# Kernel tuning notes

Hardware: AMD Instinct MI355X
Metric: run time of the kernel (lower is better)

Reference implementation:

```python
import jax, jax.numpy as jnp
import numpy as np

B, T, I, H = 64, 256, 512, 1024


def setup_inputs() -> dict:
    key = jax.random.key(0)
    ks = jax.random.split(key, 7)
    sI = 1.0 / np.sqrt(I)
    sH = 1.0 / np.sqrt(H)
    x = jax.random.normal(ks[0], (B, T, I), dtype=jnp.float32)
    # Gate order along axis 0: f, i, c(g), o. Each Linear has weight + bias.
    W_x = jax.random.normal(ks[1], (4, H, I), dtype=jnp.float32) * sI   # Wfx,Wix,Wcx,Wox weights
    b_x = jax.random.normal(ks[2], (4, H), dtype=jnp.float32) * sI      # their biases
    W_h = jax.random.normal(ks[3], (4, H, H), dtype=jnp.float32) * sH   # WfH,WiH,WcH,WoH weights
    b_h = jax.random.normal(ks[4], (4, H), dtype=jnp.float32) * sH      # their biases
    # Bf/Bi/Bc/Bo are nn.Linear(1, H) applied to a constant scalar 1.0:
    # B*(1) = weight[:, 0] + bias  -> just two extra [4, H] bias vectors.
    w_B = jax.random.normal(ks[5], (4, H), dtype=jnp.float32)
    b_B = jax.random.normal(ks[6], (4, H), dtype=jnp.float32)
    return {"x": x, "W_x": W_x, "b_x": b_x, "W_h": W_h, "b_h": b_h, "w_B": w_B, "b_B": b_B}


def reference(x, W_x, b_x, W_h, b_h, w_B, b_B):
    Bb, Tt, Ii = x.shape
    Hh = W_h.shape[-1]
    # All input-dependent gate pre-activations and all static biases, precomputed
    # in one batched GEMM: [B, T, 4, H]
    bias = b_x + b_h + w_B + b_B                     # [4, H]
    xg = jnp.einsum('bti,ghi->btgh', x, W_x) + bias  # [B, T, 4, H]

    h0 = jnp.zeros((Bb, Hh), dtype=x.dtype)
    c0 = jnp.zeros((Bb, Hh), dtype=x.dtype)

    def step(carry, xg_t):
        h, c = carry
        g = xg_t + jnp.einsum('bh,gkh->bgk', h, W_h)  # [B, 4, H]
        f = jax.nn.sigmoid(g[:, 0])
        i = jax.nn.sigmoid(g[:, 1])
        g_c = jnp.tanh(g[:, 2])
        o = jax.nn.sigmoid(g[:, 3])
        c_new = f * c + i * g_c
        h_new = o * jnp.tanh(c_new)
        return (h_new, c_new), h_new

    (_, _), hs = jax.lax.scan(step, (h0, c0), jnp.swapaxes(xg, 0, 1))  # hs: [T, B, H]
    return jnp.swapaxes(hs, 0, 1)  # [B, T, H]
```

## Files before the change

kernel.cpp:

```cpp
#include <hip/hip_runtime.h>
#include <hip/hip_cooperative_groups.h>

namespace cg = cooperative_groups;


using f32x4 = __attribute__((ext_vector_type(4))) float;
using u32x4 = __attribute__((ext_vector_type(4))) unsigned int;

#define NB 64
#define NT 256
#define NI 512
#define NH 1024

#define OFF_WHH  0u
#define SZ_WHH   (4u*1024u*1024u*2u)
#define OFF_WXH  (OFF_WHH + SZ_WHH)
#define SZ_WXH   (4u*1024u*512u*2u)
#define OFF_XH   (OFF_WXH + SZ_WXH)
#define SZ_XH    (256u*64u*512u*2u)
#define OFF_BIAS (OFF_XH + SZ_XH)
#define SZ_BIAS  (4096u*4u)
#define OFF_HG   (OFF_BIAS + SZ_BIAS)
#define SZ_HG    (2u*4u*16u*1024u*2u)
#define OFF_FLG  (OFF_HG + SZ_HG)
#define SZ_FLG   (256u*4u*64u*4u)
#define OFF_XG   (OFF_FLG + SZ_FLG)
#define SZ_XG    (256ull*64ull*4ull*1024ull*2ull)

#define L_H    0
#define L_WX   32768
#define L_ACC_S  98304
#define L_HOUT_S 102656
#define LDS_SLOW 103168
#define L_ACC_F  32768
#define L_HOUT_F 37120
#define LDS_FAST 37632
#define XG_LDS   65536

#define GUARD_PRE(acc)  asm volatile("s_nop 1\ns_nop 1" : "+v"(acc))
#define GUARD_POST(acc) asm volatile("s_nop 7\ns_nop 7\ns_nop 7" : "+v"(acc))

__device__ __forceinline__ unsigned short f2h(float f) {
  _Float16 h = (_Float16)f;
  return __builtin_bit_cast(unsigned short, h);
}
__device__ __forceinline__ float h2f(unsigned short u) {
  _Float16 h = __builtin_bit_cast(_Float16, u);
  return (float)h;
}
__device__ __forceinline__ float sigmoid_f(float x) {
  return 1.0f / (1.0f + __expf(-x));
}
__device__ __forceinline__ float tanh_f(float x) {
  float xc = fminf(fmaxf(x, -15.0f), 15.0f);
  float e = __expf(2.0f * xc);
  return 1.0f - 2.0f / (e + 1.0f);
}


__global__ __launch_bounds__(256) void pack_w_kernel(
    const float* __restrict__ Wh, const float* __restrict__ Wx,
    unsigned short* __restrict__ WhP, unsigned short* __restrict__ WxP) {
  int base = (blockIdx.x * 256 + threadIdx.x) * 4;
  const int nWh = 4 * 1024 * 1024;
  const int nWx = 4 * 1024 * 512;
  if (base < nWh) {
    const float* s = Wh + base;
    unsigned int o0 = (unsigned int)f2h(s[0]) | ((unsigned int)f2h(s[1]) << 16);
    unsigned int o1 = (unsigned int)f2h(s[2]) | ((unsigned int)f2h(s[3]) << 16);
    ((unsigned int*)(WhP + base))[0] = o0;
    ((unsigned int*)(WhP + base))[1] = o1;
  } else {
    int b2 = base - nWh;
    if (b2 < nWx) {
      const float* s = Wx + b2;
      unsigned int o0 = (unsigned int)f2h(s[0]) | ((unsigned int)f2h(s[1]) << 16);
      unsigned int o1 = (unsigned int)f2h(s[2]) | ((unsigned int)f2h(s[3]) << 16);
      ((unsigned int*)(WxP + b2))[0] = o0;
      ((unsigned int*)(WxP + b2))[1] = o1;
    }
  }
}

__global__ __launch_bounds__(256) void pack_x_kernel(
    const float* __restrict__ x, unsigned short* __restrict__ xh) {
  int gid = blockIdx.x * 256 + threadIdx.x;
  int i8 = gid & 63;
  int t  = (gid >> 6) & 255;
  int b  = gid >> 14;
  const float* s = x + (((size_t)b * NT + t) * NI + i8 * 8);
  unsigned int w[4];
#pragma unroll
  for (int j = 0; j < 4; ++j)
    w[j] = (unsigned int)f2h(s[2*j]) | ((unsigned int)f2h(s[2*j+1]) << 16);
  u32x4 v = {w[0], w[1], w[2], w[3]};
  *(u32x4*)(xh + (((size_t)t * NB + b) * NI + i8 * 8)) = v;
}

__global__ __launch_bounds__(256) void prep_small_kernel(
    const float* __restrict__ b_x, const float* __restrict__ b_h,
    const float* __restrict__ w_B, const float* __restrict__ b_B,
    float* __restrict__ bias) {
  int gid = blockIdx.x * 256 + threadIdx.x;
  if (gid < 4096) bias[gid] = b_x[gid] + b_h[gid] + w_B[gid] + b_B[gid];
}


__global__ __launch_bounds__(256) void xg_gemm(
    const unsigned short* __restrict__ Wxh,
    const unsigned short* __restrict__ xh,
    unsigned short* __restrict__ xg) {
  extern __shared__ char smem[];
  const int ug = blockIdx.x & 63;
  const int mc = blockIdx.x >> 6;
  const int tid  = threadIdx.x;
  const int w    = tid >> 6;
  const int l15  = tid & 15;
  const int kg   = (tid & 63) >> 4;

  {
    int r = tid >> 2, seg = tid & 3;
    int gg = r >> 4, uu = r & 15;
    const unsigned short* wsrc = Wxh + ((size_t)(gg * 1024 + ug * 16 + uu)) * 512;
    char* row = smem + r * 1024;
    int sw = (r & 7) << 4;
#pragma unroll
    for (int j = 0; j < 16; ++j) {
      int chunk = seg * 16 + j;
      u32x4 v = *(const u32x4*)(wsrc + chunk * 8);
      *(u32x4*)(row + ((chunk * 16) ^ sw)) = v;
    }
  }
  __syncthreads();

  const int swl = (l15 & 7) << 4;

#pragma unroll 1
  for (int i = 0; i < 4; ++i) {
    const int mt = mc * 16 + w * 4 + i;
    const int t  = mt >> 2;
    const int b0 = (mt & 3) << 4;

    u32x4 xa[16];
    const unsigned short* xp = xh + ((size_t)t * NB + b0 + l15) * NI + kg * 8;
#pragma unroll
    for (int kc = 0; kc < 16; ++kc) xa[kc] = *(const u32x4*)(xp + kc * 32);

#pragma unroll 1
    for (int gg = 0; gg < 4; ++gg) {
      f32x4 acc = {0.0f, 0.0f, 0.0f, 0.0f};
      GUARD_PRE(acc);
      const char* wxrow = smem + (gg * 16 + l15) * 1024;
#pragma unroll
      for (int kc = 0; kc < 16; ++kc) {
        u32x4 b = *(const u32x4*)(wxrow + ((kc * 64 + kg * 16) ^ swl));
        asm("v_mfma_f32_16x16x32_f16 %0, %1, %2, %0" : "+v"(acc) : "v"(xa[kc]), "v"(b));
      }
      GUARD_POST(acc);

#pragma unroll
      for (int r = 0; r < 4; ++r) {
        size_t addr = (((size_t)t * NB + b0 + kg * 4 + r) * 4 + gg) * 1024 + ug * 16 + l15;
        xg[addr] = f2h(acc[r]);
      }
    }
  }
}


__global__ __launch_bounds__(256, 1) void lstm_persist_slow(
    const unsigned short* __restrict__ Whh,
    const unsigned short* __restrict__ Wxh,
    const unsigned short* __restrict__ xh,
    const float* __restrict__ bias,
    unsigned short* __restrict__ hglob,
    unsigned int* __restrict__ flags,
    float* __restrict__ out) {
  extern __shared__ char smem[];
  const int bid  = blockIdx.x;
  const int bt   = bid & 3;
  const int ug   = bid >> 2;
  const int tid  = threadIdx.x;
  const int g    = tid >> 6;
  const int lane = tid & 63;
  const int l15  = lane & 15;
  const int kg   = lane >> 4;

  cg::grid_group grid = cg::this_grid();

  __hip_atomic_store(&flags[bid * 256 + tid], 0u,
                     __ATOMIC_RELAXED, __HIP_MEMORY_SCOPE_AGENT);

  u32x4 bh[32];
  {
    const unsigned short* wr = Whh + ((size_t)(g * 1024 + ug * 16 + l15)) * 1024 + kg * 8;
#pragma unroll
    for (int kc = 0; kc < 32; ++kc) bh[kc] = *(const u32x4*)(wr + kc * 32);
  }
#pragma unroll
  for (int kc = 0; kc < 32; ++kc)
    asm volatile("" : "+v"(bh[kc]));
  {
    int r = tid >> 2, seg = tid & 3;
    int gg = r >> 4, uu = r & 15;
    const unsigned short* wsrc = Wxh + ((size_t)(gg * 1024 + ug * 16 + uu)) * 512;
    char* row = smem + L_WX + r * 1024;
    int sw = (r & 7) << 4;
#pragma unroll
    for (int j = 0; j < 16; ++j) {
      int chunk = seg * 16 + j;
      u32x4 v = *(const u32x4*)(wsrc + chunk * 8);
      *(u32x4*)(row + ((chunk * 16) ^ sw)) = v;
    }
  }
  const float bv = bias[g * 1024 + ug * 16 + l15];
  __syncthreads();

  grid.sync();

  const int eb = tid >> 4;
  const int eu = tid & 15;
  float c_reg = 0.0f;

  float* accl = (float*)(smem + L_ACC_S);
  unsigned short* houtl = (unsigned short*)(smem + L_HOUT_S);

  for (int t = 0; t < NT; ++t) {
    const int buf = t & 1, pbuf = buf ^ 1;

    f32x4 acc = {bv, bv, bv, bv};
    GUARD_PRE(acc);

    {
      const unsigned short* xp = xh + ((size_t)t * NB + bt * 16 + l15) * NI + kg * 8;
      const char* wxrow = smem + L_WX + (g * 16 + l15) * 1024;
      const int sw = (l15 & 7) << 4;
#pragma unroll
      for (int kc = 0; kc < 16; ++kc) {
        u32x4 a = *(const u32x4*)(xp + kc * 32);
        u32x4 b = *(const u32x4*)(wxrow + ((kc * 64 + kg * 16) ^ sw));
        asm("v_mfma_f32_16x16x32_f16 %0, %1, %2, %0" : "+v"(acc) : "v"(a), "v"(b));
      }
    }

    if (t > 0) {
      if (g == 0) {
        const unsigned int* cp = flags + ((t - 1) * 4 + bt) * 64 + lane;
        unsigned int fv;
        while (true) {
          asm volatile("global_load_dword %0, %1, off sc0 sc1\n\ts_waitcnt vmcnt(0)"
                       : "=v"(fv) : "v"(cp) : "memory");
          if (__all(fv == 1u)) break;
          __builtin_amdgcn_s_sleep(2);
        }
      }
      __syncthreads();

      const int sb = tid >> 4, sc = tid & 15;
      const unsigned short* hp = hglob + ((size_t)(pbuf * 4 + bt) * 16 + sb) * 1024 + sc * 8;
      u32x4 v0, v1, v2, v3, v4, v5, v6, v7;
      asm volatile(
          "global_load_dwordx4 %0, %[p], off sc0 sc1\n\t"
          "global_load_dwordx4 %1, %[p], off offset:256 sc0 sc1\n\t"
          "global_load_dwordx4 %2, %[p], off offset:512 sc0 sc1\n\t"
          "global_load_dwordx4 %3, %[p], off offset:768 sc0 sc1\n\t"
          "global_load_dwordx4 %4, %[p], off offset:1024 sc0 sc1\n\t"
          "global_load_dwordx4 %5, %[p], off offset:1280 sc0 sc1\n\t"
          "global_load_dwordx4 %6, %[p], off offset:1536 sc0 sc1\n\t"
          "global_load_dwordx4 %7, %[p], off offset:1792 sc0 sc1\n\t"
          "s_waitcnt vmcnt(0)"
          : "=&v"(v0), "=&v"(v1), "=&v"(v2), "=&v"(v3),
            "=&v"(v4), "=&v"(v5), "=&v"(v6), "=&v"(v7)
          : [p] "v"(hp)
          : "memory");
      char* hrow = smem + L_H + sb * 2048;
      const int sw = (sb & 7) << 4;
      *(u32x4*)(hrow + ((sc * 16 +    0) ^ sw)) = v0;
      *(u32x4*)(hrow + ((sc * 16 +  256) ^ sw)) = v1;
      *(u32x4*)(hrow + ((sc * 16 +  512) ^ sw)) = v2;
      *(u32x4*)(hrow + ((sc * 16 +  768) ^ sw)) = v3;
      *(u32x4*)(hrow + ((sc * 16 + 1024) ^ sw)) = v4;
      *(u32x4*)(hrow + ((sc * 16 + 1280) ^ sw)) = v5;
      *(u32x4*)(hrow + ((sc * 16 + 1536) ^ sw)) = v6;
      *(u32x4*)(hrow + ((sc * 16 + 1792) ^ sw)) = v7;
      __syncthreads();

      const char* hbase = smem + L_H + l15 * 2048;
      const int swh = (l15 & 7) << 4;
#pragma unroll
      for (int kc = 0; kc < 32; ++kc) {
        u32x4 a = *(const u32x4*)(hbase + ((kc * 64 + kg * 16) ^ swh));
        asm("v_mfma_f32_16x16x32_f16 %0, %1, %2, %0" : "+v"(acc) : "v"(a), "v"(bh[kc]));
      }
    }
    GUARD_POST(acc);

#pragma unroll
    for (int r = 0; r < 4; ++r)
      accl[g * 272 + (kg * 4 + r) * 17 + l15] = acc[r];
    __syncthreads();

    {
      float gf = accl[0 * 272 + eb * 17 + eu];
      float gi = accl[1 * 272 + eb * 17 + eu];
      float gc = accl[2 * 272 + eb * 17 + eu];
      float go = accl[3 * 272 + eb * 17 + eu];
      float f  = sigmoid_f(gf);
      float i  = sigmoid_f(gi);
      float cb = tanh_f(gc);
      float o  = sigmoid_f(go);
      float cn = f * c_reg + i * cb;
      c_reg = cn;
      float hn = o * tanh_f(cn);
      out[(((size_t)(bt * 16 + eb)) * NT + t) * NH + ug * 16 + eu] = hn;
      houtl[eb * 16 + eu] = f2h(hn);
    }
    __syncthreads();

    if (t + 1 < NT) {
      if (tid < 32) {
        u32x4 hv = *(const u32x4*)(houtl + tid * 8);
        unsigned short* dst = hglob + ((size_t)(buf * 4 + bt) * 16 + (tid >> 1)) * 1024
                            + ug * 16 + (tid & 1) * 8;
        asm volatile("global_store_dwordx4 %[p], %[v], off sc0 sc1\n\t"
                     "s_waitcnt vmcnt(0)"
                     :: [p] "v"(dst), [v] "v"(hv) : "memory");
      }
      if (tid == 0) {
        unsigned int* fp = flags + (t * 4 + bt) * 64 + ug;
        unsigned int one = 1u;
        asm volatile("global_store_dword %0, %1, off sc0 sc1"
                     :: "v"(fp), "v"(one) : "memory");
      }
    }
  }
}


__global__ __launch_bounds__(256, 1) void lstm_persist_fast(
    const unsigned short* __restrict__ Whh,
    const unsigned short* __restrict__ xg,
    const float* __restrict__ bias,
    unsigned short* __restrict__ hglob,
    unsigned int* __restrict__ flags,
    float* __restrict__ out) {
  extern __shared__ char smem[];
  const int bid  = blockIdx.x;
  const int bt   = bid & 3;
  const int ug   = bid >> 2;
  const int tid  = threadIdx.x;
  const int g    = tid >> 6;
  const int lane = tid & 63;
  const int l15  = lane & 15;
  const int kg   = lane >> 4;

  cg::grid_group grid = cg::this_grid();

  __hip_atomic_store(&flags[bid * 256 + tid], 0u,
                     __ATOMIC_RELAXED, __HIP_MEMORY_SCOPE_AGENT);

  u32x4 bh[32];
  {
    const unsigned short* wr = Whh + ((size_t)(g * 1024 + ug * 16 + l15)) * 1024 + kg * 8;
#pragma unroll
    for (int kc = 0; kc < 32; ++kc) bh[kc] = *(const u32x4*)(wr + kc * 32);
  }
#pragma unroll
  for (int kc = 0; kc < 32; ++kc)
    asm volatile("" : "+v"(bh[kc]));
  const float bv = bias[g * 1024 + ug * 16 + l15];
  __syncthreads();

  grid.sync();

  const int eb = tid >> 4;
  const int eu = tid & 15;
  float c_reg = 0.0f;

  float* accl = (float*)(smem + L_ACC_F);
  unsigned short* houtl = (unsigned short*)(smem + L_HOUT_F);

  const size_t xg_eb = ((size_t)(bt * 16 + eb) * 4) * 1024 + ug * 16 + eu;
  const size_t xg_tstr = (size_t)NB * 4 * 1024;

  for (int t = 0; t < NT; ++t) {
    const int buf = t & 1, pbuf = buf ^ 1;

    const unsigned short* qp = xg + (size_t)t * xg_tstr + xg_eb;
    unsigned short q0 = qp[0];
    unsigned short q1 = qp[1024];
    unsigned short q2 = qp[2048];
    unsigned short q3 = qp[3072];

    f32x4 acc = {bv, bv, bv, bv};
    GUARD_PRE(acc);

    if (t > 0) {
      if (g == 0) {
        const unsigned int* cp = flags + ((t - 1) * 4 + bt) * 64 + lane;
        unsigned int fv;
        while (true) {
          asm volatile("global_load_dword %0, %1, off sc0 sc1\n\ts_waitcnt vmcnt(0)"
                       : "=v"(fv) : "v"(cp) : "memory");
          if (__all(fv == 1u)) break;
          __builtin_amdgcn_s_sleep(2);
        }
      }
      __syncthreads();

      const int sb = tid >> 4, sc = tid & 15;
      const unsigned short* hp = hglob + ((size_t)(pbuf * 4 + bt) * 16 + sb) * 1024 + sc * 8;
      u32x4 v0, v1, v2, v3, v4, v5, v6, v7;
      asm volatile(
          "global_load_dwordx4 %0, %[p], off sc0 sc1\n\t"
          "global_load_dwordx4 %1, %[p], off offset:256 sc0 sc1\n\t"
          "global_load_dwordx4 %2, %[p], off offset:512 sc0 sc1\n\t"
          "global_load_dwordx4 %3, %[p], off offset:768 sc0 sc1\n\t"
          "global_load_dwordx4 %4, %[p], off offset:1024 sc0 sc1\n\t"
          "global_load_dwordx4 %5, %[p], off offset:1280 sc0 sc1\n\t"
          "global_load_dwordx4 %6, %[p], off offset:1536 sc0 sc1\n\t"
          "global_load_dwordx4 %7, %[p], off offset:1792 sc0 sc1\n\t"
          "s_waitcnt vmcnt(0)"
          : "=&v"(v0), "=&v"(v1), "=&v"(v2), "=&v"(v3),
            "=&v"(v4), "=&v"(v5), "=&v"(v6), "=&v"(v7)
          : [p] "v"(hp)
          : "memory");
      char* hrow = smem + L_H + sb * 2048;
      const int sw = (sb & 7) << 4;
      *(u32x4*)(hrow + ((sc * 16 +    0) ^ sw)) = v0;
      *(u32x4*)(hrow + ((sc * 16 +  256) ^ sw)) = v1;
      *(u32x4*)(hrow + ((sc * 16 +  512) ^ sw)) = v2;
      *(u32x4*)(hrow + ((sc * 16 +  768) ^ sw)) = v3;
      *(u32x4*)(hrow + ((sc * 16 + 1024) ^ sw)) = v4;
      *(u32x4*)(hrow + ((sc * 16 + 1280) ^ sw)) = v5;
      *(u32x4*)(hrow + ((sc * 16 + 1536) ^ sw)) = v6;
      *(u32x4*)(hrow + ((sc * 16 + 1792) ^ sw)) = v7;
      __syncthreads();

      const char* hbase = smem + L_H + l15 * 2048;
      const int swh = (l15 & 7) << 4;
#pragma unroll
      for (int kc = 0; kc < 32; ++kc) {
        u32x4 a = *(const u32x4*)(hbase + ((kc * 64 + kg * 16) ^ swh));
        asm("v_mfma_f32_16x16x32_f16 %0, %1, %2, %0" : "+v"(acc) : "v"(a), "v"(bh[kc]));
      }
    }
    GUARD_POST(acc);

#pragma unroll
    for (int r = 0; r < 4; ++r)
      accl[g * 272 + (kg * 4 + r) * 17 + l15] = acc[r];
    __syncthreads();

    {
      float gf = accl[0 * 272 + eb * 17 + eu] + h2f(q0);
      float gi = accl[1 * 272 + eb * 17 + eu] + h2f(q1);
      float gc = accl[2 * 272 + eb * 17 + eu] + h2f(q2);
      float go = accl[3 * 272 + eb * 17 + eu] + h2f(q3);
      float f  = sigmoid_f(gf);
      float i  = sigmoid_f(gi);
      float cb = tanh_f(gc);
      float o  = sigmoid_f(go);
      float cn = f * c_reg + i * cb;
      c_reg = cn;
      float hn = o * tanh_f(cn);
      out[(((size_t)(bt * 16 + eb)) * NT + t) * NH + ug * 16 + eu] = hn;
      houtl[eb * 16 + eu] = f2h(hn);
    }
    __syncthreads();

    if (t + 1 < NT) {
      if (tid < 32) {
        u32x4 hv = *(const u32x4*)(houtl + tid * 8);
        unsigned short* dst = hglob + ((size_t)(buf * 4 + bt) * 16 + (tid >> 1)) * 1024
                            + ug * 16 + (tid & 1) * 8;
        asm volatile("global_store_dwordx4 %[p], %[v], off sc0 sc1\n\t"
                     "s_waitcnt vmcnt(0)"
                     :: [p] "v"(dst), [v] "v"(hv) : "memory");
      }
      if (tid == 0) {
        unsigned int* fp = flags + (t * 4 + bt) * 64 + ug;
        unsigned int one = 1u;
        asm volatile("global_store_dword %0, %1, off sc0 sc1"
                     :: "v"(fp), "v"(one) : "memory");
      }
    }
  }
}


extern "C" void kernel_launch(void* const* d_in, const int* in_sizes, int n_in,
                              void* d_out, int out_size, void* d_ws, size_t ws_size,
                              hipStream_t stream) {
  (void)in_sizes; (void)n_in; (void)out_size;
  const float* x   = (const float*)d_in[0];
  const float* W_x = (const float*)d_in[1];
  const float* b_x = (const float*)d_in[2];
  const float* W_h = (const float*)d_in[3];
  const float* b_h = (const float*)d_in[4];
  const float* w_B = (const float*)d_in[5];
  const float* b_B = (const float*)d_in[6];
  float* out = (float*)d_out;

  char* ws = (char*)d_ws;
  unsigned short* Whh  = (unsigned short*)(ws + OFF_WHH);
  unsigned short* Wxh  = (unsigned short*)(ws + OFF_WXH);
  unsigned short* xhp  = (unsigned short*)(ws + OFF_XH);
  float*          bias = (float*)(ws + OFF_BIAS);
  unsigned short* hg   = (unsigned short*)(ws + OFF_HG);
  unsigned int*   flg  = (unsigned int*)(ws + OFF_FLG);
  unsigned short* xg   = (unsigned short*)(ws + OFF_XG);

  const size_t need_fast = (size_t)OFF_XG + (size_t)SZ_XG;
  const bool fast = (ws_size >= need_fast);

  hipFuncSetAttribute(reinterpret_cast<const void*>(lstm_persist_slow),
                      hipFuncAttributeMaxDynamicSharedMemorySize, LDS_SLOW);
  hipFuncSetAttribute(reinterpret_cast<const void*>(lstm_persist_fast),
                      hipFuncAttributeMaxDynamicSharedMemorySize, LDS_FAST);
  hipFuncSetAttribute(reinterpret_cast<const void*>(xg_gemm),
                      hipFuncAttributeMaxDynamicSharedMemorySize, XG_LDS);

  pack_w_kernel<<<dim3(6144), dim3(256), 0, stream>>>(W_h, W_x, Whh, Wxh);
  pack_x_kernel<<<dim3(4096), dim3(256), 0, stream>>>(x, xhp);
  prep_small_kernel<<<dim3(16), dim3(256), 0, stream>>>(b_x, b_h, w_B, b_B, bias);

  if (fast) {
    xg_gemm<<<dim3(4096), dim3(256), XG_LDS, stream>>>(Wxh, xhp, xg);
    void* kargs[] = {(void*)&Whh, (void*)&xg, (void*)&bias,
                     (void*)&hg, (void*)&flg, (void*)&out};
    hipLaunchCooperativeKernel(reinterpret_cast<void*>(lstm_persist_fast),
                               dim3(256), dim3(256), kargs, LDS_FAST, stream);
  } else {
    void* kargs[] = {(void*)&Whh, (void*)&Wxh, (void*)&xhp, (void*)&bias,
                     (void*)&hg, (void*)&flg, (void*)&out};
    hipLaunchCooperativeKernel(reinterpret_cast<void*>(lstm_persist_slow),
                               dim3(256), dim3(256), kargs, LDS_SLOW, stream);
  }
}
```

Baseline: 1.096 ms.

## Widen xg GEMM tiles to 32 units and split recurrent MFMA accumulator chain

The input-projection GEMM now gives each block 32 hidden units instead of 16, staging 128KB of W_x in LDS and halving the grid, so each loaded x fragment feeds twice as many MFMAs. Separately, the recurrent step in the persistent fast kernel splits its 32-deep MFMA dependency chain across two accumulators that are summed at the end, to shorten the serial MFMA latency on the critical per-timestep path. The larger LDS footprint lowers xg_gemm occupancy, and the two-accumulator sum changes the rounding order slightly.

Measured after the change: 1.184 ms. +8.0%, slower.

```diff
diff --git a/kernel.cpp b/kernel.cpp
--- a/kernel.cpp
+++ b/kernel.cpp
@@ -35,7 +35,7 @@
 #define L_ACC_F  32768
 #define L_HOUT_F 37120
 #define LDS_FAST 37632
-#define XG_LDS   65536
+#define XG_LDS   131072
 
 #define GUARD_PRE(acc)  asm volatile("s_nop 1\ns_nop 1" : "+v"(acc))
 #define GUARD_POST(acc) asm volatile("s_nop 7\ns_nop 7\ns_nop 7" : "+v"(acc))
@@ -111,22 +111,22 @@
     const unsigned short* __restrict__ xh,
     unsigned short* __restrict__ xg) {
   extern __shared__ char smem[];
-  const int ug = blockIdx.x & 63;
-  const int mc = blockIdx.x >> 6;
+  const int ug2 = blockIdx.x & 31;
+  const int mc  = blockIdx.x >> 5;
   const int tid  = threadIdx.x;
   const int w    = tid >> 6;
   const int l15  = tid & 15;
   const int kg   = (tid & 63) >> 4;
 
   {
-    int r = tid >> 2, seg = tid & 3;
-    int gg = r >> 4, uu = r & 15;
-    const unsigned short* wsrc = Wxh + ((size_t)(gg * 1024 + ug * 16 + uu)) * 512;
-    char* row = smem + r * 1024;
-    int sw = (r & 7) << 4;
-#pragma unroll
-    for (int j = 0; j < 16; ++j) {
-      int chunk = seg * 16 + j;
+    int rr = tid >> 1, seg = tid & 1;
+    int gg = rr >> 5, uu = rr & 31;
+    const unsigned short* wsrc = Wxh + ((size_t)(gg * 1024 + ug2 * 32 + uu)) * 512;
+    char* row = smem + rr * 1024;
+    int sw = (rr & 7) << 4;
+#pragma unroll
+    for (int j = 0; j < 32; ++j) {
+      int chunk = seg * 32 + j;
       u32x4 v = *(const u32x4*)(wsrc + chunk * 8);
       *(u32x4*)(row + ((chunk * 16) ^ sw)) = v;
     }
@@ -148,20 +148,24 @@
 
 #pragma unroll 1
     for (int gg = 0; gg < 4; ++gg) {
-      f32x4 acc = {0.0f, 0.0f, 0.0f, 0.0f};
-      GUARD_PRE(acc);
-      const char* wxrow = smem + (gg * 16 + l15) * 1024;
-#pragma unroll
-      for (int kc = 0; kc < 16; ++kc) {
-        u32x4 b = *(const u32x4*)(wxrow + ((kc * 64 + kg * 16) ^ swl));
-        asm("v_mfma_f32_16x16x32_f16 %0, %1, %2, %0" : "+v"(acc) : "v"(xa[kc]), "v"(b));
-      }
-      GUARD_POST(acc);
-
-#pragma unroll
-      for (int r = 0; r < 4; ++r) {
-        size_t addr = (((size_t)t * NB + b0 + kg * 4 + r) * 4 + gg) * 1024 + ug * 16 + l15;
-        xg[addr] = f2h(acc[r]);
+#pragma unroll 1
+      for (int us = 0; us < 2; ++us) {
+        f32x4 acc = {0.0f, 0.0f, 0.0f, 0.0f};
+        GUARD_PRE(acc);
+        const char* wxrow = smem + (gg * 32 + us * 16 + l15) * 1024;
+#pragma unroll
+        for (int kc = 0; kc < 16; ++kc) {
+          u32x4 b = *(const u32x4*)(wxrow + ((kc * 64 + kg * 16) ^ swl));
+          asm("v_mfma_f32_16x16x32_f16 %0, %1, %2, %0" : "+v"(acc) : "v"(xa[kc]), "v"(b));
+        }
+        GUARD_POST(acc);
+
+#pragma unroll
+        for (int r = 0; r < 4; ++r) {
+          size_t addr = (((size_t)t * NB + b0 + kg * 4 + r) * 4 + gg) * 1024
+                      + ug2 * 32 + us * 16 + l15;
+          xg[addr] = f2h(acc[r]);
+        }
       }
     }
   }
@@ -392,8 +396,10 @@
     unsigned short q2 = qp[2048];
     unsigned short q3 = qp[3072];
 
-    f32x4 acc = {bv, bv, bv, bv};
-    GUARD_PRE(acc);
+    f32x4 accA = {bv, bv, bv, bv};
+    f32x4 accB = {0.0f, 0.0f, 0.0f, 0.0f};
+    GUARD_PRE(accA);
+    GUARD_PRE(accB);
 
     if (t > 0) {
       if (g == 0) {
@@ -440,16 +446,19 @@
       const char* hbase = smem + L_H + l15 * 2048;
       const int swh = (l15 & 7) << 4;
 #pragma unroll
-      for (int kc = 0; kc < 32; ++kc) {
-        u32x4 a = *(const u32x4*)(hbase + ((kc * 64 + kg * 16) ^ swh));
-        asm("v_mfma_f32_16x16x32_f16 %0, %1, %2, %0" : "+v"(acc) : "v"(a), "v"(bh[kc]));
-      }
-    }
-    GUARD_POST(acc);
+      for (int kc = 0; kc < 32; kc += 2) {
+        u32x4 a0 = *(const u32x4*)(hbase + (((kc    ) * 64 + kg * 16) ^ swh));
+        u32x4 a1 = *(const u32x4*)(hbase + (((kc + 1) * 64 + kg * 16) ^ swh));
+        asm("v_mfma_f32_16x16x32_f16 %0, %1, %2, %0" : "+v"(accA) : "v"(a0), "v"(bh[kc]));
+        asm("v_mfma_f32_16x16x32_f16 %0, %1, %2, %0" : "+v"(accB) : "v"(a1), "v"(bh[kc + 1]));
+      }
+    }
+    GUARD_POST(accA);
+    GUARD_POST(accB);
 
 #pragma unroll
     for (int r = 0; r < 4; ++r)
-      accl[g * 272 + (kg * 4 + r) * 17 + l15] = acc[r];
+      accl[g * 272 + (kg * 4 + r) * 17 + l15] = accA[r] + accB[r];
     __syncthreads();
 
     {
@@ -526,7 +535,7 @@
   prep_small_kernel<<<dim3(16), dim3(256), 0, stream>>>(b_x, b_h, w_B, b_B, bias);
 
   if (fast) {
-    xg_gemm<<<dim3(4096), dim3(256), XG_LDS, stream>>>(Wxh, xhp, xg);
+    xg_gemm<<<dim3(2048), dim3(256), XG_LDS, stream>>>(Wxh, xhp, xg);
     void* kargs[] = {(void*)&Whh, (void*)&xg, (void*)&bias,
                      (void*)&hg, (void*)&flg, (void*)&out};
     hipLaunchCooperativeKernel(reinterpret_cast<void*>(lstm_persist_fast),
```
